# Kernel optimization log

Measured on AMD Instinct MI355X. Metric: run time of the kernel, lower is better.

The kernel has to match this reference:

```python
import jax, jax.numpy as jnp
import numpy as np

NEG_INF = -jnp.inf  # aggregation identity for the max-plus semifield


def setup_inputs() -> dict:
    key = jax.random.key(0)
    k1, k2, k3 = jax.random.split(key, 3)
    B, C_in, C_out, H, W, M, N = 4, 32, 32, 80, 80, 5, 5
    x = jax.random.normal(k1, (B, C_in, H, W), dtype=jnp.float32)
    w = jax.random.normal(k2, (C_out, C_in, M, N), dtype=jnp.float32) * 0.1
    bias = jax.random.normal(k3, (C_out,), dtype=jnp.float32) * 0.1
    return {"x": x, "w": w, "bias": bias}


def reference(x, w, bias):
    """Max-plus semifield conv: out[b,co,h,w] = bias[co] + sum_ci max_{m,n} (x_pad[b,ci,h+m,w+n] + w[co,ci,m,n]).

    Faithful to SemiConv2d._semi_conv with semifield = (amax, add, -inf, 0),
    but computed with a running max over the MN taps instead of materializing
    the [B, C_out, C_in, M*N, H*W] tensor the torch code builds via unfold.
    """
    B, C_in, H, W = x.shape
    C_out, _, M, N = w.shape
    # padding exactly as in _semi_conv (odd vs even kernel), fill = aggregation identity
    pt, pb = (M // 2, M // 2) if M % 2 else (M // 2 - 1, M // 2)
    pl, pr = (N // 2, N // 2) if N % 2 else (N // 2 - 1, N // 2)
    xp = jnp.pad(x, ((0, 0), (0, 0), (pt, pb), (pl, pr)), constant_values=NEG_INF)
    # running max over the M*N taps (fixed small loop, not a data-dim loop)
    acc = jnp.full((B, C_out, C_in, H, W), NEG_INF, dtype=x.dtype)
    for m in range(M):
        for n in range(N):
            patch = xp[:, :, m:m + H, n:n + W]               # [B, C_in, H, W]
            tap = patch[:, None] + w[None, :, :, m, n, None, None]  # [B, C_out, C_in, H, W]
            acc = jnp.maximum(acc, tap)
    out = jnp.sum(acc, axis=2) + bias[None, :, None, None]   # sum over C_in, add bias
    return out
```

## Files before the change

kernel.cpp:

```cpp
#include <hip/hip_runtime.h>
#include <math.h>

#define CIN  32
#define COUT 32
#define BB   4
#define HH   80
#define WW   80
#define HW   (HH * WW)
#define NOUT (BB * COUT * HW)
#define TH   16
#define XROWS (TH + 4)
#define XCOLS (WW + 4)
#define TILE  (XROWS * XCOLS)
#define TILEP 1696
#define NTHREADS 320

template<int NPARTS>
__global__ __launch_bounds__(NTHREADS, 6) void semiconv_kernel(
    const float* __restrict__ x,
    const float* __restrict__ w,
    const float* __restrict__ bias,
    float* __restrict__ dst)
{
    constexpr int CIP = CIN / NPARTS;
    __shared__ __align__(16) float xs[2][TILEP];
    __shared__ __align__(16) float wl[CIP * 28];

    const int tid = threadIdx.x;
    const int bh  = blockIdx.x;
    const int co  = blockIdx.y;
    const int zz  = blockIdx.z;
    const int b    = zz / NPARTS;
    const int part = zz % NPARTS;
    const int ci0  = part * CIP;
    const int h0   = bh * TH;

    for (int idx = tid; idx < CIP * 28; idx += NTHREADS) {
        int ci = idx / 28, k = idx % 28;
        wl[idx] = (k < 25) ? w[((co * CIN) + ci0 + ci) * 25 + k] : 0.0f;
    }

    const int ty = tid / 20;
    const int tx = tid % 20;
    const int wc = tx * 4;

    int goff[6], lidx[6];
    #pragma unroll
    for (int i = 0; i < 6; ++i) {
        int idx = tid + i * NTHREADS;
        int r = idx / XCOLS, c = idx % XCOLS;
        int gr = h0 + r - 2, gc = c - 2;
        lidx[i] = idx;
        goff[i] = (gr >= 0 && gr < HH && gc >= 0 && gc < WW) ? (gr * WW + gc) : -1;
    }
    const bool has6 = (tid < TILE - 5 * NTHREADS);

    float pre[6];
    auto prefetch = [&](int ci) {
        const float* xp = x + (size_t)(b * CIN + ci) * HW;
        #pragma unroll
        for (int i = 0; i < 5; ++i)
            pre[i] = (goff[i] >= 0) ? xp[goff[i]] : -INFINITY;
        if (has6) pre[5] = (goff[5] >= 0) ? xp[goff[5]] : -INFINITY;
    };

    prefetch(ci0);
    float sum0 = 0.f, sum1 = 0.f, sum2 = 0.f, sum3 = 0.f;
    int buf = 0;

    for (int k = 0; k < CIP; ++k) {
        float* xb = xs[buf];
        #pragma unroll
        for (int i = 0; i < 5; ++i) xb[lidx[i]] = pre[i];
        if (has6) xb[lidx[5]] = pre[5];
        __syncthreads();
        if (k + 1 < CIP) prefetch(ci0 + k + 1);

        const float* wk = &wl[k * 28];
        float mx0 = -INFINITY, mx1 = -INFINITY, mx2 = -INFINITY, mx3 = -INFINITY;
        #pragma unroll
        for (int m = 0; m < 5; ++m) {
            const float4* rowp = reinterpret_cast<const float4*>(&xb[(ty + m) * XCOLS + wc]);
            float4 a = rowp[0], c4 = rowp[1];
            float x0=a.x, x1=a.y, x2=a.z, x3=a.w, x4=c4.x, x5=c4.y, x6=c4.z, x7=c4.w;
            float w0=wk[m*5+0], w1=wk[m*5+1], w2=wk[m*5+2], w3=wk[m*5+3], w4=wk[m*5+4];

            float t0 = fmaxf(fmaxf(x0 + w0, x1 + w1), x2 + w2);
            t0 = fmaxf(fmaxf(t0, x3 + w3), x4 + w4);
            mx0 = fmaxf(mx0, t0);
            float t1 = fmaxf(fmaxf(x1 + w0, x2 + w1), x3 + w2);
            t1 = fmaxf(fmaxf(t1, x4 + w3), x5 + w4);
            mx1 = fmaxf(mx1, t1);
            float t2 = fmaxf(fmaxf(x2 + w0, x3 + w1), x4 + w2);
            t2 = fmaxf(fmaxf(t2, x5 + w3), x6 + w4);
            mx2 = fmaxf(mx2, t2);
            float t3 = fmaxf(fmaxf(x3 + w0, x4 + w1), x5 + w2);
            t3 = fmaxf(fmaxf(t3, x6 + w3), x7 + w4);
            mx3 = fmaxf(mx3, t3);
        }
        sum0 += mx0; sum1 += mx1; sum2 += mx2; sum3 += mx3;
        buf ^= 1;
    }

    size_t oi = (((size_t)b * COUT + co) * HH + (h0 + ty)) * WW + wc;
    float4 r;
    if (NPARTS == 1) {
        const float bc = bias[co];
        r.x = sum0 + bc; r.y = sum1 + bc; r.z = sum2 + bc; r.w = sum3 + bc;
    } else {
        r.x = sum0; r.y = sum1; r.z = sum2; r.w = sum3;
        oi += (size_t)part * NOUT;
    }
    *reinterpret_cast<float4*>(dst + oi) = r;
}

__global__ __launch_bounds__(256) void reduce2_kernel(
    const float* __restrict__ ws, const float* __restrict__ bias,
    float* __restrict__ out)
{
    int i4 = blockIdx.x * 256 + threadIdx.x;
    const float4* p0 = reinterpret_cast<const float4*>(ws);
    const float4* p1 = p0 + (NOUT / 4);
    float4 a = p0[i4], c = p1[i4];
    int co = (i4 / (HW / 4)) & (COUT - 1);
    float bc = bias[co];
    float4 r;
    r.x = a.x + c.x + bc; r.y = a.y + c.y + bc;
    r.z = a.z + c.z + bc; r.w = a.w + c.w + bc;
    reinterpret_cast<float4*>(out)[i4] = r;
}

extern "C" void kernel_launch(void* const* d_in, const int* in_sizes, int n_in,
                              void* d_out, int out_size, void* d_ws, size_t ws_size,
                              hipStream_t stream) {
    const float* x    = (const float*)d_in[0];
    const float* w    = (const float*)d_in[1];
    const float* bias = (const float*)d_in[2];
    float* out        = (float*)d_out;

    const size_t need = 2ull * NOUT * sizeof(float);
    if (ws_size >= need) {
        dim3 grid(HH / TH, COUT, BB * 2);
        semiconv_kernel<2><<<grid, NTHREADS, 0, stream>>>(x, w, bias, (float*)d_ws);
        reduce2_kernel<<<NOUT / 4 / 256, 256, 0, stream>>>((const float*)d_ws, bias, out);
    } else {
        dim3 grid(HH / TH, COUT, BB);
        semiconv_kernel<1><<<grid, NTHREADS, 0, stream>>>(x, w, bias, out);
    }
}
```

Baseline: 38.48 us.

## Compute two output channels per block and split input channels four ways

Each block now produces two output channels from the same shared-memory input tile, so each x tile load and LDS read serves twice the arithmetic. Weights are read straight from global memory into registers each iteration, no longer staged in LDS. When workspace allows, the input-channel split grows from 2 to 4 parts, which keeps the grid large enough, and a generic N-way reduction kernel sums the partials. The cost is more register pressure (occupancy hint lowered to 4), four times the workspace traffic for partials, and uniform global weight loads inside the loop.

After: 42.63 us. +10.8%, slower.

```diff
diff --git a/kernel.cpp b/kernel.cpp
--- a/kernel.cpp
+++ b/kernel.cpp
@@ -9,51 +9,44 @@
 #define HW   (HH * WW)
 #define NOUT (BB * COUT * HW)
 #define TH   16
-#define XROWS (TH + 4)
-#define XCOLS (WW + 4)
-#define TILE  (XROWS * XCOLS)
-#define TILEP 1696
-#define NTHREADS 320
+#define XR   (TH + 4)
+#define XC   (WW + 4)
+#define TILE (XR * XC)
+#define NT   320
 
 template<int NPARTS>
-__global__ __launch_bounds__(NTHREADS, 6) void semiconv_kernel(
+__global__ __launch_bounds__(NT, 4) void semiconv_kernel(
     const float* __restrict__ x,
     const float* __restrict__ w,
     const float* __restrict__ bias,
     float* __restrict__ dst)
 {
     constexpr int CIP = CIN / NPARTS;
-    __shared__ __align__(16) float xs[2][TILEP];
-    __shared__ __align__(16) float wl[CIP * 28];
+    __shared__ __align__(16) float xs[2][TILE];
 
     const int tid = threadIdx.x;
     const int bh  = blockIdx.x;
-    const int co  = blockIdx.y;
+    const int cp  = blockIdx.y;
     const int zz  = blockIdx.z;
     const int b    = zz / NPARTS;
     const int part = zz % NPARTS;
     const int ci0  = part * CIP;
     const int h0   = bh * TH;
-
-    for (int idx = tid; idx < CIP * 28; idx += NTHREADS) {
-        int ci = idx / 28, k = idx % 28;
-        wl[idx] = (k < 25) ? w[((co * CIN) + ci0 + ci) * 25 + k] : 0.0f;
-    }
+    const int co0  = cp * 2;
 
     const int ty = tid / 20;
     const int tx = tid % 20;
     const int wc = tx * 4;
 
-    int goff[6], lidx[6];
+    int goff[6];
     #pragma unroll
     for (int i = 0; i < 6; ++i) {
-        int idx = tid + i * NTHREADS;
-        int r = idx / XCOLS, c = idx % XCOLS;
+        int idx = tid + i * NT;
+        int r = idx / XC, c = idx % XC;
         int gr = h0 + r - 2, gc = c - 2;
-        lidx[i] = idx;
         goff[i] = (gr >= 0 && gr < HH && gc >= 0 && gc < WW) ? (gr * WW + gc) : -1;
     }
-    const bool has6 = (tid < TILE - 5 * NTHREADS);
+    const bool has6 = (tid < TILE - 5 * NT);
 
     float pre[6];
     auto prefetch = [&](int ci) {
@@ -64,69 +57,88 @@
         if (has6) pre[5] = (goff[5] >= 0) ? xp[goff[5]] : -INFINITY;
     };
 
+    const float* wp0 = w + ((size_t)(co0    ) * CIN + ci0) * 25;
+    const float* wp1 = w + ((size_t)(co0 + 1) * CIN + ci0) * 25;
+
     prefetch(ci0);
-    float sum0 = 0.f, sum1 = 0.f, sum2 = 0.f, sum3 = 0.f;
+    float s0a=0.f,s1a=0.f,s2a=0.f,s3a=0.f;
+    float s0b=0.f,s1b=0.f,s2b=0.f,s3b=0.f;
     int buf = 0;
 
     for (int k = 0; k < CIP; ++k) {
+        float w0[25], w1[25];
+        #pragma unroll
+        for (int j = 0; j < 25; ++j) { w0[j] = wp0[k * 25 + j]; w1[j] = wp1[k * 25 + j]; }
+
         float* xb = xs[buf];
         #pragma unroll
-        for (int i = 0; i < 5; ++i) xb[lidx[i]] = pre[i];
-        if (has6) xb[lidx[5]] = pre[5];
+        for (int i = 0; i < 5; ++i) xb[tid + i * NT] = pre[i];
+        if (has6) xb[tid + 5 * NT] = pre[5];
         __syncthreads();
         if (k + 1 < CIP) prefetch(ci0 + k + 1);
 
-        const float* wk = &wl[k * 28];
-        float mx0 = -INFINITY, mx1 = -INFINITY, mx2 = -INFINITY, mx3 = -INFINITY;
+        float a0=-INFINITY,a1=-INFINITY,a2=-INFINITY,a3=-INFINITY;
+        float b0=-INFINITY,b1=-INFINITY,b2=-INFINITY,b3=-INFINITY;
         #pragma unroll
         for (int m = 0; m < 5; ++m) {
-            const float4* rowp = reinterpret_cast<const float4*>(&xb[(ty + m) * XCOLS + wc]);
-            float4 a = rowp[0], c4 = rowp[1];
-            float x0=a.x, x1=a.y, x2=a.z, x3=a.w, x4=c4.x, x5=c4.y, x6=c4.z, x7=c4.w;
-            float w0=wk[m*5+0], w1=wk[m*5+1], w2=wk[m*5+2], w3=wk[m*5+3], w4=wk[m*5+4];
-
-            float t0 = fmaxf(fmaxf(x0 + w0, x1 + w1), x2 + w2);
-            t0 = fmaxf(fmaxf(t0, x3 + w3), x4 + w4);
-            mx0 = fmaxf(mx0, t0);
-            float t1 = fmaxf(fmaxf(x1 + w0, x2 + w1), x3 + w2);
-            t1 = fmaxf(fmaxf(t1, x4 + w3), x5 + w4);
-            mx1 = fmaxf(mx1, t1);
-            float t2 = fmaxf(fmaxf(x2 + w0, x3 + w1), x4 + w2);
-            t2 = fmaxf(fmaxf(t2, x5 + w3), x6 + w4);
-            mx2 = fmaxf(mx2, t2);
-            float t3 = fmaxf(fmaxf(x3 + w0, x4 + w1), x5 + w2);
-            t3 = fmaxf(fmaxf(t3, x6 + w3), x7 + w4);
-            mx3 = fmaxf(mx3, t3);
+            const float4* rp = reinterpret_cast<const float4*>(&xb[(ty + m) * XC + wc]);
+            float4 A = rp[0], C = rp[1];
+            float x0=A.x,x1=A.y,x2=A.z,x3=A.w,x4=C.x,x5=C.y,x6=C.z,x7=C.w;
+            {
+                float q0=w0[5*m],q1=w0[5*m+1],q2=w0[5*m+2],q3=w0[5*m+3],q4=w0[5*m+4];
+                float t, u;
+                t=fmaxf(fmaxf(x0+q0,x1+q1),x2+q2); u=fmaxf(x3+q3,x4+q4); a0=fmaxf(fmaxf(a0,t),u);
+                t=fmaxf(fmaxf(x1+q0,x2+q1),x3+q2); u=fmaxf(x4+q3,x5+q4); a1=fmaxf(fmaxf(a1,t),u);
+                t=fmaxf(fmaxf(x2+q0,x3+q1),x4+q2); u=fmaxf(x5+q3,x6+q4); a2=fmaxf(fmaxf(a2,t),u);
+                t=fmaxf(fmaxf(x3+q0,x4+q1),x5+q2); u=fmaxf(x6+q3,x7+q4); a3=fmaxf(fmaxf(a3,t),u);
+            }
+            {
+                float q0=w1[5*m],q1=w1[5*m+1],q2=w1[5*m+2],q3=w1[5*m+3],q4=w1[5*m+4];
+                float t, u;
+                t=fmaxf(fmaxf(x0+q0,x1+q1),x2+q2); u=fmaxf(x3+q3,x4+q4); b0=fmaxf(fmaxf(b0,t),u);
+                t=fmaxf(fmaxf(x1+q0,x2+q1),x3+q2); u=fmaxf(x4+q3,x5+q4); b1=fmaxf(fmaxf(b1,t),u);
+                t=fmaxf(fmaxf(x2+q0,x3+q1),x4+q2); u=fmaxf(x5+q3,x6+q4); b2=fmaxf(fmaxf(b2,t),u);
+                t=fmaxf(fmaxf(x3+q0,x4+q1),x5+q2); u=fmaxf(x6+q3,x7+q4); b3=fmaxf(fmaxf(b3,t),u);
+            }
         }
-        sum0 += mx0; sum1 += mx1; sum2 += mx2; sum3 += mx3;
+        s0a+=a0; s1a+=a1; s2a+=a2; s3a+=a3;
+        s0b+=b0; s1b+=b1; s2b+=b2; s3b+=b3;
         buf ^= 1;
     }
 
-    size_t oi = (((size_t)b * COUT + co) * HH + (h0 + ty)) * WW + wc;
-    float4 r;
+    size_t oiA = (((size_t)b * COUT + co0    ) * HH + (h0 + ty)) * WW + wc;
+    size_t oiB = (((size_t)b * COUT + co0 + 1) * HH + (h0 + ty)) * WW + wc;
+    float4 rA, rB;
     if (NPARTS == 1) {
-        const float bc = bias[co];
-        r.x = sum0 + bc; r.y = sum1 + bc; r.z = sum2 + bc; r.w = sum3 + bc;
+        const float bcA = bias[co0], bcB = bias[co0 + 1];
+        rA.x=s0a+bcA; rA.y=s1a+bcA; rA.z=s2a+bcA; rA.w=s3a+bcA;
+        rB.x=s0b+bcB; rB.y=s1b+bcB; rB.z=s2b+bcB; rB.w=s3b+bcB;
     } else {
-        r.x = sum0; r.y = sum1; r.z = sum2; r.w = sum3;
-        oi += (size_t)part * NOUT;
+        rA.x=s0a; rA.y=s1a; rA.z=s2a; rA.w=s3a;
+        rB.x=s0b; rB.y=s1b; rB.z=s2b; rB.w=s3b;
+        oiA += (size_t)part * NOUT;
+        oiB += (size_t)part * NOUT;
     }
-    *reinterpret_cast<float4*>(dst + oi) = r;
+    *reinterpret_cast<float4*>(dst + oiA) = rA;
+    *reinterpret_cast<float4*>(dst + oiB) = rB;
 }
 
-__global__ __launch_bounds__(256) void reduce2_kernel(
+template<int NPARTS>
+__global__ __launch_bounds__(256) void reduceN_kernel(
     const float* __restrict__ ws, const float* __restrict__ bias,
     float* __restrict__ out)
 {
     int i4 = blockIdx.x * 256 + threadIdx.x;
-    const float4* p0 = reinterpret_cast<const float4*>(ws);
-    const float4* p1 = p0 + (NOUT / 4);
-    float4 a = p0[i4], c = p1[i4];
+    const float4* p = reinterpret_cast<const float4*>(ws);
+    float4 r = p[i4];
+    #pragma unroll
+    for (int q = 1; q < NPARTS; ++q) {
+        float4 t = p[i4 + (size_t)q * (NOUT / 4)];
+        r.x += t.x; r.y += t.y; r.z += t.z; r.w += t.w;
+    }
     int co = (i4 / (HW / 4)) & (COUT - 1);
     float bc = bias[co];
-    float4 r;
-    r.x = a.x + c.x + bc; r.y = a.y + c.y + bc;
-    r.z = a.z + c.z + bc; r.w = a.w + c.w + bc;
+    r.x += bc; r.y += bc; r.z += bc; r.w += bc;
     reinterpret_cast<float4*>(out)[i4] = r;
 }
 
@@ -138,13 +150,19 @@
     const float* bias = (const float*)d_in[2];
     float* out        = (float*)d_out;
 
-    const size_t need = 2ull * NOUT * sizeof(float);
-    if (ws_size >= need) {
-        dim3 grid(HH / TH, COUT, BB * 2);
-        semiconv_kernel<2><<<grid, NTHREADS, 0, stream>>>(x, w, bias, (float*)d_ws);
-        reduce2_kernel<<<NOUT / 4 / 256, 256, 0, stream>>>((const float*)d_ws, bias, out);
+    const size_t need4 = 4ull * NOUT * sizeof(float);
+    const size_t need2 = 2ull * NOUT * sizeof(float);
+
+    if (ws_size >= need4) {
+        dim3 grid(HH / TH, COUT / 2, BB * 4);
+        semiconv_kernel<4><<<grid, NT, 0, stream>>>(x, w, bias, (float*)d_ws);
+        reduceN_kernel<4><<<NOUT / 4 / 256, 256, 0, stream>>>((const float*)d_ws, bias, out);
+    } else if (ws_size >= need2) {
+        dim3 grid(HH / TH, COUT / 2, BB * 2);
+        semiconv_kernel<2><<<grid, NT, 0, stream>>>(x, w, bias, (float*)d_ws);
+        reduceN_kernel<2><<<NOUT / 4 / 256, 256, 0, stream>>>((const float*)d_ws, bias, out);
     } else {
-        dim3 grid(HH / TH, COUT, BB);
-        semiconv_kernel<1><<<grid, NTHREADS, 0, stream>>>(x, w, bias, out);
+        dim3 grid(HH / TH, COUT / 2, BB);
+        semiconv_kernel<1><<<grid, NT, 0, stream>>>(x, w, bias, out);
     }
 }
```
